# Kernel optimization log

Hardware: AMD Instinct MI355X
Metric: run time of the kernel (lower is better)

## Reference

```python
import jax, jax.numpy as jnp
import numpy as np

N, H, E, H1, H2, S = 64, 128, 32, 128, 64, 4096
U, I, L = 32, 32, 16
D = U + I + L + S + 2 * S  # linear input dim = num_features + 2*num_skills
P = H * (H - 1) // 2
# strictly-lower-triangular pair indices, row-major (i, j<i) -- matches the torch mask order
I_IDX, J_IDX = np.tril_indices(H, -1)
I_IDX = jnp.asarray(I_IDX)
J_IDX = jnp.asarray(J_IDX)


def setup_inputs() -> dict:
    key = jax.random.key(0)
    ks = jax.random.split(key, 16)
    skills = jax.random.randint(ks[0], (N, H), 1, S)  # avoid padding idx 0 for realism
    targets = jax.random.bernoulli(ks[1], 0.5, (N, H)).astype(jnp.float32)
    users = jax.random.normal(ks[2], (N, U), jnp.float32)
    items = jax.random.normal(ks[3], (N * H, I), jnp.float32)
    langs = jax.random.normal(ks[4], (N * H, L), jnp.float32)
    mask = jax.random.bernoulli(ks[5], 0.8, (N * H,))
    emb_table = (0.02 * jax.random.normal(ks[6], (S, E), jnp.float32)).at[0].set(0.0)  # padding_idx=0
    W1 = 0.05 * jax.random.normal(ks[7], (2 * E, H1), jnp.float32)
    b1 = jnp.zeros((H1,), jnp.float32)
    W2 = 0.05 * jax.random.normal(ks[8], (H1, H2), jnp.float32)
    b2 = jnp.zeros((H2,), jnp.float32)
    Ws = 0.05 * jax.random.normal(ks[9], (H2, 1), jnp.float32)
    bs = jnp.zeros((1,), jnp.float32)
    Wlin = 0.01 * jax.random.normal(ks[10], (D, 1), jnp.float32)
    blin = jnp.zeros((1,), jnp.float32)
    return dict(skills=skills, targets=targets, users=users, items=items, langs=langs,
                mask=mask, emb_table=emb_table, W1=W1, b1=b1, W2=W2, b2=b2,
                Ws=Ws, bs=bs, Wlin=Wlin, blin=blin)


def reference(skills, targets, users, items, langs, mask,
              emb_table, W1, b1, W2, b2, Ws, bs, Wlin, blin):
    # ---- compute_correct_total ----
    emb = emb_table[skills]                      # [N, H, E] gather
    e_i = emb[:, I_IDX]                          # current skill emb per pair [N, P, E]
    e_j = emb[:, J_IDX]                          # history skill emb per pair [N, P, E]
    x = jnp.concatenate([e_i, e_j], axis=-1)     # [N, P, 2E]
    h = jax.nn.relu(x @ W1 + b1)                 # dropout = 0 (eval)
    h = jax.nn.relu(h @ W2 + b2)
    sim = jnp.tanh(h @ Ws + bs)[..., 0]          # [N, P]
    # per-position segment sums: seg[n, i] = sum_{j<i} sim[n, (i,j)]
    seg_total = jnp.zeros((N, H), jnp.float32).at[:, I_IDX].add(sim)
    sim_correct = sim * targets[:, J_IDX]        # weight by history correctness
    seg_correct = jnp.zeros((N, H), jnp.float32).at[:, I_IDX].add(sim_correct)
    # per-skill scatter-add into dense [N, 2S] feature tensor
    rows = jnp.arange(N)[:, None]
    tcf = (jnp.zeros((N, 2 * S), jnp.float32)
           .at[rows, skills].add(seg_total)
           .at[rows, skills + S].add(seg_correct))
    # ---- forward ----
    onehot = jax.nn.one_hot(skills.reshape(-1), S, dtype=jnp.float32)   # [N*H, S]
    feats = jnp.concatenate([
        jnp.repeat(users, H, axis=0),            # repeat_interleave over seq positions
        items, langs, onehot,
        jnp.repeat(tcf, H, axis=0),
    ], axis=1)                                   # [N*H, D]
    logits = feats @ Wlin + blin                 # [N*H, 1]
    z = logits.reshape(-1)
    y = targets.reshape(-1)
    m = mask.astype(jnp.float32)
    # masked mean BCE-with-logits (z_weight = 0)
    bce = jnp.maximum(z, 0.0) - z * y + jnp.log1p(jnp.exp(-jnp.abs(z)))
    loss = jnp.sum(bce * m) / jnp.maximum(jnp.sum(m), 1.0)
    return loss, jax.nn.sigmoid(logits)
```

## Files before the change

kernel.cpp:

```cpp
#include <hip/hip_runtime.h>
#include <hip/hip_fp16.h>

#define N_ 64
#define H_ 128
#define E_ 32
#define H1_ 128
#define H2_ 64
#define S_ 4096
#define OFF_ITEMS 32
#define OFF_LANGS 64
#define OFF_ONEHOT 80
#define OFF_TCF 4176
#define OFF_TCF2 8272

typedef _Float16 half8 __attribute__((ext_vector_type(8)));
typedef short short8 __attribute__((ext_vector_type(8)));
typedef float floatx4 __attribute__((ext_vector_type(4)));

__global__ __launch_bounds__(256) void pair_mlp_fused(
    const int* __restrict__ skills, const float* __restrict__ emb_table,
    const float* __restrict__ W1, const float* __restrict__ b1,
    const float* __restrict__ W2, const float* __restrict__ targets,
    const float* __restrict__ b2, const float* __restrict__ Ws,
    const float* __restrict__ bs,
    float* __restrict__ segP, float* __restrict__ accums_region) {

    int bid = blockIdx.x;
    int tid = threadIdx.x;

    if (bid == 0 && tid < 4) accums_region[tid] = 0.f;

    int n = bid / 10;
    int t = bid % 10;
    int ti = 0;
    while ((ti + 1) * (ti + 2) / 2 <= t) ti++;
    int tj = t - ti * (ti + 1) / 2;
    int i0 = ti * 32, j0 = tj * 32;
    bool diag = (ti == tj);

    __shared__ __align__(16) _Float16 aL[32][136];
    __shared__ __align__(16) _Float16 bL[32][136];
    __shared__ float tgt[32];
    __shared__ float sT[32], sC[32];

    int lane = tid & 63, wv = tid >> 6;
    int hi = lane >> 4, lo = lane & 15;

    bool isA = (wv < 2);
    int rbase = (isA ? i0 : j0) + (wv & 1) * 16;
    int woff = isA ? 0 : 32;

    int sk = skills[n * H_ + rbase + lo];
    float4 e0 = *(const float4*)(emb_table + (size_t)sk * 32 + 8 * hi);
    float4 e1 = *(const float4*)(emb_table + (size_t)sk * 32 + 8 * hi + 4);
    half8 afrag;
    afrag[0] = (_Float16)e0.x; afrag[1] = (_Float16)e0.y;
    afrag[2] = (_Float16)e0.z; afrag[3] = (_Float16)e0.w;
    afrag[4] = (_Float16)e1.x; afrag[5] = (_Float16)e1.y;
    afrag[6] = (_Float16)e1.z; afrag[7] = (_Float16)e1.w;

    {
        _Float16 (*dst)[136] = isA ? aL : bL;
        int rloc0 = (wv & 1) * 16 + 4 * hi;
        #pragma unroll
        for (int ct = 0; ct < 8; ct++) {
            float cinit = isA ? b1[16 * ct + lo] : 0.f;
            floatx4 accB = (floatx4){cinit, cinit, cinit, cinit};
            half8 bf;
            #pragma unroll
            for (int e = 0; e < 8; e++)
                bf[e] = (_Float16)W1[(woff + 8 * hi + e) * 128 + 16 * ct + lo];
            accB = __builtin_amdgcn_mfma_f32_16x16x32_f16(afrag, bf, accB, 0, 0, 0);
            #pragma unroll
            for (int q = 0; q < 4; q++)
                dst[rloc0 + q][16 * ct + lo] = (_Float16)accB[q];
        }
    }

    if (tid < 32) {
        tgt[tid] = targets[n * H_ + j0 + tid];
        sT[tid] = 0.f;
        sC[tid] = 0.f;
    }

    half8 wfrag[4][4];
    #pragma unroll
    for (int kk = 0; kk < 4; kk++)
        #pragma unroll
        for (int nt = 0; nt < 4; nt++) {
            half8 wf;
            #pragma unroll
            for (int e = 0; e < 8; e++)
                wf[e] = (_Float16)W2[(32 * kk + 8 * hi + e) * 64 + 16 * nt + lo];
            wfrag[kk][nt] = wf;
        }

    float b2v[4], wsv[4];
    #pragma unroll
    for (int nt = 0; nt < 4; nt++) {
        b2v[nt] = b2[16 * nt + lo];
        wsv[nt] = Ws[16 * nt + lo];
    }
    float bsv = bs[0];

    __syncthreads();

    for (int g = wv; g < 64; g += 4) {
        int li = g >> 1;
        int hf = g & 1;
        if (diag && li <= 16 * hf) continue;

        const _Float16* arow = &aL[li][0];
        const _Float16* brow = &bL[16 * hf + lo][0];

        floatx4 acc[4];
        #pragma unroll
        for (int nt = 0; nt < 4; nt++) acc[nt] = (floatx4){0.f, 0.f, 0.f, 0.f};

        #pragma unroll
        for (int kk = 0; kk < 4; kk++) {
            half8 av = *(const half8*)(arow + 32 * kk + 8 * hi);
            half8 bv = *(const half8*)(brow + 32 * kk + 8 * hi);
            half8 s = av + bv;
            short8 bits = __builtin_bit_cast(short8, s);
            short8 sgn = bits >> 15;
            bits &= ~sgn;
            half8 h = __builtin_bit_cast(half8, bits);
            acc[0] = __builtin_amdgcn_mfma_f32_16x16x32_f16(h, wfrag[kk][0], acc[0], 0, 0, 0);
            acc[1] = __builtin_amdgcn_mfma_f32_16x16x32_f16(h, wfrag[kk][1], acc[1], 0, 0, 0);
            acc[2] = __builtin_amdgcn_mfma_f32_16x16x32_f16(h, wfrag[kk][2], acc[2], 0, 0, 0);
            acc[3] = __builtin_amdgcn_mfma_f32_16x16x32_f16(h, wfrag[kk][3], acc[3], 0, 0, 0);
        }

        float part[4];
        #pragma unroll
        for (int r4 = 0; r4 < 4; r4++) {
            float p = 0.f;
            #pragma unroll
            for (int nt = 0; nt < 4; nt++)
                p += fmaxf(acc[nt][r4] + b2v[nt], 0.f) * wsv[nt];
            part[r4] = p;
        }
        #pragma unroll
        for (int m = 1; m <= 8; m <<= 1) {
            #pragma unroll
            for (int r4 = 0; r4 < 4; r4++)
                part[r4] += __shfl_xor(part[r4], m, 64);
        }
        float sumT = 0.f, sumC = 0.f;
        #pragma unroll
        for (int r4 = 0; r4 < 4; r4++) {
            int srow = 4 * hi + r4;
            int lj = 16 * hf + srow;
            bool valid = (!diag) || (li > lj);
            float x = part[r4] + bsv;
            float e2 = __expf(2.f * x);
            float sv = (e2 - 1.f) / (e2 + 1.f);
            sv = valid ? sv : 0.f;
            sumT += sv;
            sumC += sv * tgt[lj];
        }
        if (lo == 0) {
            atomicAdd(&sT[li], sumT);
            atomicAdd(&sC[li], sumC);
        }
    }

    __syncthreads();
    if (tid < 32) {
        segP[(size_t)bid * 64 + tid]      = sT[tid];
        segP[(size_t)bid * 64 + 32 + tid] = sC[tid];
    }
}

__global__ void finalize(const int* __restrict__ skills,
                         const float* __restrict__ targets,
                         const float* __restrict__ users,
                         const float* __restrict__ items,
                         const float* __restrict__ langs,
                         const void* __restrict__ mask,
                         const float* __restrict__ Wlin,
                         const float* __restrict__ blin,
                         const float* __restrict__ segP,
                         float* __restrict__ out,
                         float* __restrict__ accums,
                         int* __restrict__ counter) {
    int n = blockIdx.x, h = threadIdx.x;
    int nh = n * H_ + h;
    int sk = skills[nh];

    const unsigned* mw = (const unsigned*)mask;
    bool byte_layout = false;
    #pragma unroll
    for (int q = 0; q < 16; q++) byte_layout |= (mw[q] > 1u);
    float m = byte_layout ? (((const unsigned char*)mask)[nh] ? 1.f : 0.f)
                          : (mw[nh] ? 1.f : 0.f);

    int ti = h >> 5, r = h & 31;
    int tb = ti * (ti + 1) / 2;
    float sT = 0.f, sC = 0.f;
    for (int tj = 0; tj <= ti; tj++) {
        const float* p = segP + (size_t)(n * 10 + tb + tj) * 64;
        sT += p[r];
        sC += p[32 + r];
    }

    float tterm = sT * Wlin[OFF_TCF + sk] + sC * Wlin[OFF_TCF2 + sk];
    if (h < 32) tterm += users[n * 32 + h] * Wlin[h];

    __shared__ float cred[2];
    {
        float v = tterm;
        #pragma unroll
        for (int mm = 1; mm <= 32; mm <<= 1) v += __shfl_xor(v, mm, 64);
        if ((h & 63) == 0) cred[h >> 6] = v;
    }
    __syncthreads();
    float c = cred[0] + cred[1] + blin[0];

    float z = c + Wlin[OFF_ONEHOT + sk];
    const float4* ip = (const float4*)(items + (size_t)nh * 32);
    #pragma unroll
    for (int i4 = 0; i4 < 8; i4++) {
        float4 v = ip[i4];
        z += v.x * Wlin[OFF_ITEMS + 4 * i4]     + v.y * Wlin[OFF_ITEMS + 4 * i4 + 1]
           + v.z * Wlin[OFF_ITEMS + 4 * i4 + 2] + v.w * Wlin[OFF_ITEMS + 4 * i4 + 3];
    }
    const float4* lp = (const float4*)(langs + (size_t)nh * 16);
    #pragma unroll
    for (int l4 = 0; l4 < 4; l4++) {
        float4 v = lp[l4];
        z += v.x * Wlin[OFF_LANGS + 4 * l4]     + v.y * Wlin[OFF_LANGS + 4 * l4 + 1]
           + v.z * Wlin[OFF_LANGS + 4 * l4 + 2] + v.w * Wlin[OFF_LANGS + 4 * l4 + 3];
    }

    out[1 + nh] = 1.f / (1.f + __expf(-z));

    float y = targets[nh];
    float bce = fmaxf(z, 0.f) - z * y + log1pf(__expf(-fabsf(z)));

    __shared__ float s1[2], s2[2];
    {
        float x1 = bce * m, x2 = m;
        #pragma unroll
        for (int mm = 1; mm <= 32; mm <<= 1) {
            x1 += __shfl_xor(x1, mm, 64);
            x2 += __shfl_xor(x2, mm, 64);
        }
        if ((h & 63) == 0) { s1[h >> 6] = x1; s2[h >> 6] = x2; }
    }
    __syncthreads();
    if (h == 0) {
        atomicAdd(&accums[0], s1[0] + s1[1]);
        atomicAdd(&accums[1], s2[0] + s2[1]);
        __threadfence();
        if (atomicAdd(counter, 1) == N_ - 1) {
            float a = atomicAdd(&accums[0], 0.f);
            float b = atomicAdd(&accums[1], 0.f);
            out[0] = a / fmaxf(b, 1.f);
        }
    }
}

extern "C" void kernel_launch(void* const* d_in, const int* in_sizes, int n_in,
                              void* d_out, int out_size, void* d_ws, size_t ws_size,
                              hipStream_t stream) {
    const int*   skills  = (const int*)d_in[0];
    const float* targets = (const float*)d_in[1];
    const float* users   = (const float*)d_in[2];
    const float* items   = (const float*)d_in[3];
    const float* langs   = (const float*)d_in[4];
    const void*  mask    = (const void*)d_in[5];
    const float* emb     = (const float*)d_in[6];
    const float* W1      = (const float*)d_in[7];
    const float* b1      = (const float*)d_in[8];
    const float* W2      = (const float*)d_in[9];
    const float* b2      = (const float*)d_in[10];
    const float* Ws      = (const float*)d_in[11];
    const float* bs      = (const float*)d_in[12];
    const float* Wlin    = (const float*)d_in[13];
    const float* blin    = (const float*)d_in[14];

    char* ws = (char*)d_ws;
    float* segP    = (float*)ws;
    float* accums  = (float*)(ws + (256u << 10));
    int*   counter = (int*)(accums + 2);

    pair_mlp_fused<<<N_ * 10, 256, 0, stream>>>(skills, emb, W1, b1, W2, targets,
                                                b2, Ws, bs, segP, accums);
    finalize<<<N_, H_, 0, stream>>>(skills, targets, users, items, langs, mask,
                                    Wlin, blin, segP, (float*)d_out, accums, counter);
}
```

Measured before the change: 121.3 us.

## Fuse finalize into pair MLP via last-block-per-row ticket, stage transposed weights in LDS

Merges the finalize kernel into the pair-MLP kernel: each of the 10 tile blocks per sequence bumps a per-row counter, and the last one computes the linear logits, sigmoid and BCE for that row. A tiny zero kernel now resets the counters and accumulators. W1 and W2 are staged into shared memory as transposed fp16 with coalesced float4 loads, replacing strided scalar global loads. The second MFMA swaps its operands so each lane owns a single pair, which simplifies the reductions, and tanh uses a fast reciprocal. This trades one launch and some load inefficiency for extra LDS, more barriers and a serialized tail on the last block of each row.

```diff
diff --git a/kernel.cpp b/kernel.cpp
--- a/kernel.cpp
+++ b/kernel.cpp
@@ -17,19 +17,25 @@
 typedef short short8 __attribute__((ext_vector_type(8)));
 typedef float floatx4 __attribute__((ext_vector_type(4)));
 
-__global__ __launch_bounds__(256) void pair_mlp_fused(
+__global__ void zero_sync(float* __restrict__ zr) {
+    if (threadIdx.x < 68) zr[threadIdx.x] = 0.f;
+}
+
+__global__ __launch_bounds__(256) void fused(
     const int* __restrict__ skills, const float* __restrict__ emb_table,
     const float* __restrict__ W1, const float* __restrict__ b1,
     const float* __restrict__ W2, const float* __restrict__ targets,
+    const float* __restrict__ users, const float* __restrict__ items,
+    const float* __restrict__ langs, const void* __restrict__ mask,
     const float* __restrict__ b2, const float* __restrict__ Ws,
-    const float* __restrict__ bs,
-    float* __restrict__ segP, float* __restrict__ accums_region) {
+    const float* __restrict__ bs, const float* __restrict__ Wlin,
+    const float* __restrict__ blin,
+    float* __restrict__ segP, int* __restrict__ done,
+    float* __restrict__ accums, int* __restrict__ counter,
+    float* __restrict__ out) {
 
     int bid = blockIdx.x;
     int tid = threadIdx.x;
-
-    if (bid == 0 && tid < 4) accums_region[tid] = 0.f;
-
     int n = bid / 10;
     int t = bid % 10;
     int ti = 0;
@@ -40,16 +46,27 @@
 
     __shared__ __align__(16) _Float16 aL[32][136];
     __shared__ __align__(16) _Float16 bL[32][136];
-    __shared__ float tgt[32];
-    __shared__ float sT[32], sC[32];
+    __shared__ __align__(16) _Float16 wT[9216];
+    __shared__ float tgt[32], sT[32], sC[32];
+    __shared__ int tick_s;
+    __shared__ float cred[4], s1[4], s2[4];
 
     int lane = tid & 63, wv = tid >> 6;
     int hi = lane >> 4, lo = lane & 15;
+
+    for (int idx = tid; idx < 2048; idx += 256) {
+        int r = idx >> 5;
+        int c4 = (idx & 31) * 4;
+        float4 v = *(const float4*)(W1 + r * 128 + c4);
+        wT[(c4 + 0) * 72 + r] = (_Float16)v.x;
+        wT[(c4 + 1) * 72 + r] = (_Float16)v.y;
+        wT[(c4 + 2) * 72 + r] = (_Float16)v.z;
+        wT[(c4 + 3) * 72 + r] = (_Float16)v.w;
+    }
 
     bool isA = (wv < 2);
     int rbase = (isA ? i0 : j0) + (wv & 1) * 16;
     int woff = isA ? 0 : 32;
-
     int sk = skills[n * H_ + rbase + lo];
     float4 e0 = *(const float4*)(emb_table + (size_t)sk * 32 + 8 * hi);
     float4 e1 = *(const float4*)(emb_table + (size_t)sk * 32 + 8 * hi + 4);
@@ -59,6 +76,13 @@
     afrag[4] = (_Float16)e1.x; afrag[5] = (_Float16)e1.y;
     afrag[6] = (_Float16)e1.z; afrag[7] = (_Float16)e1.w;
 
+    if (tid < 32) {
+        tgt[tid] = targets[n * H_ + j0 + tid];
+        sT[tid] = 0.f;
+        sC[tid] = 0.f;
+    }
+    __syncthreads();
+
     {
         _Float16 (*dst)[136] = isA ? aL : bL;
         int rloc0 = (wv & 1) * 16 + 4 * hi;
@@ -66,53 +90,57 @@
         for (int ct = 0; ct < 8; ct++) {
             float cinit = isA ? b1[16 * ct + lo] : 0.f;
             floatx4 accB = (floatx4){cinit, cinit, cinit, cinit};
-            half8 bf;
-            #pragma unroll
-            for (int e = 0; e < 8; e++)
-                bf[e] = (_Float16)W1[(woff + 8 * hi + e) * 128 + 16 * ct + lo];
+            half8 bf = *(const half8*)(&wT[(16 * ct + lo) * 72 + woff + 8 * hi]);
             accB = __builtin_amdgcn_mfma_f32_16x16x32_f16(afrag, bf, accB, 0, 0, 0);
             #pragma unroll
             for (int q = 0; q < 4; q++)
                 dst[rloc0 + q][16 * ct + lo] = (_Float16)accB[q];
         }
     }
-
-    if (tid < 32) {
-        tgt[tid] = targets[n * H_ + j0 + tid];
-        sT[tid] = 0.f;
-        sC[tid] = 0.f;
-    }
-
-    half8 wfrag[4][4];
+    __syncthreads();
+
+    for (int idx = tid; idx < 2048; idx += 256) {
+        int r = idx >> 4;
+        int c4 = (idx & 15) * 4;
+        float4 v = *(const float4*)(W2 + r * 64 + c4);
+        wT[(c4 + 0) * 136 + r] = (_Float16)v.x;
+        wT[(c4 + 1) * 136 + r] = (_Float16)v.y;
+        wT[(c4 + 2) * 136 + r] = (_Float16)v.z;
+        wT[(c4 + 3) * 136 + r] = (_Float16)v.w;
+    }
+    __syncthreads();
+
+    half8 wfragT[4][4];
     #pragma unroll
     for (int kk = 0; kk < 4; kk++)
         #pragma unroll
-        for (int nt = 0; nt < 4; nt++) {
-            half8 wf;
-            #pragma unroll
-            for (int e = 0; e < 8; e++)
-                wf[e] = (_Float16)W2[(32 * kk + 8 * hi + e) * 64 + 16 * nt + lo];
-            wfrag[kk][nt] = wf;
-        }
-
-    float b2v[4], wsv[4];
+        for (int nt = 0; nt < 4; nt++)
+            wfragT[kk][nt] = *(const half8*)(&wT[(16 * nt + lo) * 136 + 32 * kk + 8 * hi]);
+
+    floatx4 b2v[4], wsv[4];
     #pragma unroll
     for (int nt = 0; nt < 4; nt++) {
-        b2v[nt] = b2[16 * nt + lo];
-        wsv[nt] = Ws[16 * nt + lo];
+        b2v[nt] = *(const floatx4*)(b2 + 16 * nt + 4 * hi);
+        wsv[nt] = *(const floatx4*)(Ws + 16 * nt + 4 * hi);
     }
     float bsv = bs[0];
 
-    __syncthreads();
+    int hf = wv & 1;
+    int lj = 16 * hf + lo;
+    half8 bfx[4];
+    {
+        const _Float16* brow = &bL[lj][0];
+        #pragma unroll
+        for (int kk = 0; kk < 4; kk++)
+            bfx[kk] = *(const half8*)(brow + 32 * kk + 8 * hi);
+    }
+    float tgtv = tgt[lj];
 
     for (int g = wv; g < 64; g += 4) {
         int li = g >> 1;
-        int hf = g & 1;
         if (diag && li <= 16 * hf) continue;
 
         const _Float16* arow = &aL[li][0];
-        const _Float16* brow = &bL[16 * hf + lo][0];
-
         floatx4 acc[4];
         #pragma unroll
         for (int nt = 0; nt < 4; nt++) acc[nt] = (floatx4){0.f, 0.f, 0.f, 0.f};
@@ -120,49 +148,40 @@
         #pragma unroll
         for (int kk = 0; kk < 4; kk++) {
             half8 av = *(const half8*)(arow + 32 * kk + 8 * hi);
-            half8 bv = *(const half8*)(brow + 32 * kk + 8 * hi);
-            half8 s = av + bv;
+            half8 s = av + bfx[kk];
             short8 bits = __builtin_bit_cast(short8, s);
             short8 sgn = bits >> 15;
             bits &= ~sgn;
             half8 h = __builtin_bit_cast(half8, bits);
-            acc[0] = __builtin_amdgcn_mfma_f32_16x16x32_f16(h, wfrag[kk][0], acc[0], 0, 0, 0);
-            acc[1] = __builtin_amdgcn_mfma_f32_16x16x32_f16(h, wfrag[kk][1], acc[1], 0, 0, 0);
-            acc[2] = __builtin_amdgcn_mfma_f32_16x16x32_f16(h, wfrag[kk][2], acc[2], 0, 0, 0);
-            acc[3] = __builtin_amdgcn_mfma_f32_16x16x32_f16(h, wfrag[kk][3], acc[3], 0, 0, 0);
-        }
-
-        float part[4];
-        #pragma unroll
-        for (int r4 = 0; r4 < 4; r4++) {
-            float p = 0.f;
+            acc[0] = __builtin_amdgcn_mfma_f32_16x16x32_f16(wfragT[kk][0], h, acc[0], 0, 0, 0);
+            acc[1] = __builtin_amdgcn_mfma_f32_16x16x32_f16(wfragT[kk][1], h, acc[1], 0, 0, 0);
+            acc[2] = __builtin_amdgcn_mfma_f32_16x16x32_f16(wfragT[kk][2], h, acc[2], 0, 0, 0);
+            acc[3] = __builtin_amdgcn_mfma_f32_16x16x32_f16(wfragT[kk][3], h, acc[3], 0, 0, 0);
+        }
+
+        float part = 0.f;
+        #pragma unroll
+        for (int nt = 0; nt < 4; nt++)
             #pragma unroll
-            for (int nt = 0; nt < 4; nt++)
-                p += fmaxf(acc[nt][r4] + b2v[nt], 0.f) * wsv[nt];
-            part[r4] = p;
-        }
+            for (int q = 0; q < 4; q++)
+                part += fmaxf(acc[nt][q] + b2v[nt][q], 0.f) * wsv[nt][q];
+        part += __shfl_xor(part, 16, 64);
+        part += __shfl_xor(part, 32, 64);
+
+        float x = part + bsv;
+        float e2 = __expf(2.f * x);
+        float sv = 1.f - 2.f * __builtin_amdgcn_rcpf(e2 + 1.f);
+        bool valid = (!diag) || (li > lj);
+        sv = valid ? sv : 0.f;
+        float svT = sv, svC = sv * tgtv;
         #pragma unroll
         for (int m = 1; m <= 8; m <<= 1) {
-            #pragma unroll
-            for (int r4 = 0; r4 < 4; r4++)
-                part[r4] += __shfl_xor(part[r4], m, 64);
-        }
-        float sumT = 0.f, sumC = 0.f;
-        #pragma unroll
-        for (int r4 = 0; r4 < 4; r4++) {
-            int srow = 4 * hi + r4;
-            int lj = 16 * hf + srow;
-            bool valid = (!diag) || (li > lj);
-            float x = part[r4] + bsv;
-            float e2 = __expf(2.f * x);
-            float sv = (e2 - 1.f) / (e2 + 1.f);
-            sv = valid ? sv : 0.f;
-            sumT += sv;
-            sumC += sv * tgt[lj];
-        }
-        if (lo == 0) {
-            atomicAdd(&sT[li], sumT);
-            atomicAdd(&sC[li], sumC);
+            svT += __shfl_xor(svT, m, 64);
+            svC += __shfl_xor(svC, m, 64);
+        }
+        if (lane == 0) {
+            atomicAdd(&sT[li], svT);
+            atomicAdd(&sC[li], svC);
         }
     }
 
@@ -171,23 +190,17 @@
         segP[(size_t)bid * 64 + tid]      = sT[tid];
         segP[(size_t)bid * 64 + 32 + tid] = sC[tid];
     }
-}
-
-__global__ void finalize(const int* __restrict__ skills,
-                         const float* __restrict__ targets,
-                         const float* __restrict__ users,
-                         const float* __restrict__ items,
-                         const float* __restrict__ langs,
-                         const void* __restrict__ mask,
-                         const float* __restrict__ Wlin,
-                         const float* __restrict__ blin,
-                         const float* __restrict__ segP,
-                         float* __restrict__ out,
-                         float* __restrict__ accums,
-                         int* __restrict__ counter) {
-    int n = blockIdx.x, h = threadIdx.x;
-    int nh = n * H_ + h;
-    int sk = skills[nh];
+    __threadfence();
+    __syncthreads();
+    if (tid == 0) tick_s = atomicAdd(&done[n], 1);
+    __syncthreads();
+    if (tick_s != 9) return;
+    __threadfence();
+
+    int h = tid;
+    bool act = h < 128;
+    int nh = n * H_ + (act ? h : 0);
+    int sk2 = skills[nh];
 
     const unsigned* mw = (const unsigned*)mask;
     bool byte_layout = false;
@@ -196,63 +209,63 @@
     float m = byte_layout ? (((const unsigned char*)mask)[nh] ? 1.f : 0.f)
                           : (mw[nh] ? 1.f : 0.f);
 
-    int ti = h >> 5, r = h & 31;
-    int tb = ti * (ti + 1) / 2;
-    float sT = 0.f, sC = 0.f;
-    for (int tj = 0; tj <= ti; tj++) {
-        const float* p = segP + (size_t)(n * 10 + tb + tj) * 64;
-        sT += p[r];
-        sC += p[32 + r];
-    }
-
-    float tterm = sT * Wlin[OFF_TCF + sk] + sC * Wlin[OFF_TCF2 + sk];
-    if (h < 32) tterm += users[n * 32 + h] * Wlin[h];
-
-    __shared__ float cred[2];
+    float tterm = 0.f, sTt = 0.f, sCt = 0.f;
+    if (act) {
+        int ti2 = h >> 5, r = h & 31;
+        int tb = ti2 * (ti2 + 1) / 2;
+        for (int tj2 = 0; tj2 <= ti2; tj2++) {
+            const float* p = segP + (size_t)(n * 10 + tb + tj2) * 64;
+            sTt += __hip_atomic_load(p + r, __ATOMIC_RELAXED, __HIP_MEMORY_SCOPE_AGENT);
+            sCt += __hip_atomic_load(p + 32 + r, __ATOMIC_RELAXED, __HIP_MEMORY_SCOPE_AGENT);
+        }
+        tterm = sTt * Wlin[OFF_TCF + sk2] + sCt * Wlin[OFF_TCF2 + sk2];
+        if (h < 32) tterm += users[n * 32 + h] * Wlin[h];
+    }
     {
         float v = tterm;
         #pragma unroll
         for (int mm = 1; mm <= 32; mm <<= 1) v += __shfl_xor(v, mm, 64);
-        if ((h & 63) == 0) cred[h >> 6] = v;
-    }
-    __syncthreads();
-    float c = cred[0] + cred[1] + blin[0];
-
-    float z = c + Wlin[OFF_ONEHOT + sk];
-    const float4* ip = (const float4*)(items + (size_t)nh * 32);
-    #pragma unroll
-    for (int i4 = 0; i4 < 8; i4++) {
-        float4 v = ip[i4];
-        z += v.x * Wlin[OFF_ITEMS + 4 * i4]     + v.y * Wlin[OFF_ITEMS + 4 * i4 + 1]
-           + v.z * Wlin[OFF_ITEMS + 4 * i4 + 2] + v.w * Wlin[OFF_ITEMS + 4 * i4 + 3];
-    }
-    const float4* lp = (const float4*)(langs + (size_t)nh * 16);
-    #pragma unroll
-    for (int l4 = 0; l4 < 4; l4++) {
-        float4 v = lp[l4];
-        z += v.x * Wlin[OFF_LANGS + 4 * l4]     + v.y * Wlin[OFF_LANGS + 4 * l4 + 1]
-           + v.z * Wlin[OFF_LANGS + 4 * l4 + 2] + v.w * Wlin[OFF_LANGS + 4 * l4 + 3];
-    }
-
-    out[1 + nh] = 1.f / (1.f + __expf(-z));
-
-    float y = targets[nh];
-    float bce = fmaxf(z, 0.f) - z * y + log1pf(__expf(-fabsf(z)));
-
-    __shared__ float s1[2], s2[2];
+        if (lane == 0) cred[wv] = v;
+    }
+    __syncthreads();
+    float c = cred[0] + cred[1] + cred[2] + cred[3] + blin[0];
+
+    float z = 0.f, bce = 0.f;
+    if (act) {
+        z = c + Wlin[OFF_ONEHOT + sk2];
+        const float4* ip = (const float4*)(items + (size_t)nh * 32);
+        #pragma unroll
+        for (int i4 = 0; i4 < 8; i4++) {
+            float4 v = ip[i4];
+            z += v.x * Wlin[OFF_ITEMS + 4 * i4]     + v.y * Wlin[OFF_ITEMS + 4 * i4 + 1]
+               + v.z * Wlin[OFF_ITEMS + 4 * i4 + 2] + v.w * Wlin[OFF_ITEMS + 4 * i4 + 3];
+        }
+        const float4* lp = (const float4*)(langs + (size_t)nh * 16);
+        #pragma unroll
+        for (int l4 = 0; l4 < 4; l4++) {
+            float4 v = lp[l4];
+            z += v.x * Wlin[OFF_LANGS + 4 * l4]     + v.y * Wlin[OFF_LANGS + 4 * l4 + 1]
+               + v.z * Wlin[OFF_LANGS + 4 * l4 + 2] + v.w * Wlin[OFF_LANGS + 4 * l4 + 3];
+        }
+        out[1 + nh] = 1.f / (1.f + __expf(-z));
+        float y = targets[nh];
+        bce = fmaxf(z, 0.f) - z * y + log1pf(__expf(-fabsf(z)));
+    }
+
     {
-        float x1 = bce * m, x2 = m;
+        float x1 = act ? bce * m : 0.f;
+        float x2 = act ? m : 0.f;
         #pragma unroll
         for (int mm = 1; mm <= 32; mm <<= 1) {
             x1 += __shfl_xor(x1, mm, 64);
             x2 += __shfl_xor(x2, mm, 64);
         }
-        if ((h & 63) == 0) { s1[h >> 6] = x1; s2[h >> 6] = x2; }
-    }
-    __syncthreads();
-    if (h == 0) {
-        atomicAdd(&accums[0], s1[0] + s1[1]);
-        atomicAdd(&accums[1], s2[0] + s2[1]);
+        if (lane == 0) { s1[wv] = x1; s2[wv] = x2; }
+    }
+    __syncthreads();
+    if (tid == 0) {
+        atomicAdd(&accums[0], s1[0] + s1[1] + s1[2] + s1[3]);
+        atomicAdd(&accums[1], s2[0] + s2[1] + s2[2] + s2[3]);
         __threadfence();
         if (atomicAdd(counter, 1) == N_ - 1) {
             float a = atomicAdd(&accums[0], 0.f);
@@ -283,11 +296,14 @@
 
     char* ws = (char*)d_ws;
     float* segP    = (float*)ws;
-    float* accums  = (float*)(ws + (256u << 10));
-    int*   counter = (int*)(accums + 2);
-
-    pair_mlp_fused<<<N_ * 10, 256, 0, stream>>>(skills, emb, W1, b1, W2, targets,
-                                                b2, Ws, bs, segP, accums);
-    finalize<<<N_, H_, 0, stream>>>(skills, targets, users, items, langs, mask,
-                                    Wlin, blin, segP, (float*)d_out, accums, counter);
+    float* syncw   = (float*)(ws + (192u << 10));
+    int*   done    = (int*)syncw;
+    float* accums  = syncw + 64;
+    int*   counter = (int*)(syncw + 66);
+
+    zero_sync<<<1, 128, 0, stream>>>(syncw);
+    fused<<<N_ * 10, 256, 0, stream>>>(skills, emb, W1, b1, W2, targets,
+                                       users, items, langs, mask,
+                                       b2, Ws, bs, Wlin, blin,
+                                       segP, done, accums, counter, (float*)d_out);
 }
```

Measured after the change: 179.1 us. 1.48x slower.
